# Optimization experiments

Measured on AMD Instinct MI355X. Metric: run time of the kernel, lower is better.

The kernel has to match this reference:

```python
import jax, jax.numpy as jnp
import numpy as np

EPS = 1e-12

def _l2n(x):
    return x / jnp.sqrt(jnp.maximum(jnp.sum(x * x, axis=-1, keepdims=True), EPS))

def _sn_kernel(w, u):
    # One power iteration of spectral normalization (TF SpectralNormalization._compute_weights).
    wr = w.reshape(-1, w.shape[-1])           # [in, out] (1x1 conv kernel flattened)
    v = _l2n(u @ wr.T)                        # [1, in]
    u2 = _l2n(v @ wr)                         # [1, out]
    u2 = jax.lax.stop_gradient(u2)
    v = jax.lax.stop_gradient(v)
    sigma = (v @ wr) @ u2.T                   # [1, 1]
    return w / sigma[0, 0]

def setup_inputs() -> dict:
    key = jax.random.key(0)
    ks = jax.random.split(key, 14)
    B, H, W, C = 8, 64, 64, 256
    d = C // 8
    inp = {
        'x':  jax.random.normal(ks[0], (B, H, W, C), jnp.float32),
        'wf': jax.random.normal(ks[1], (C, d), jnp.float32) * 0.02,
        'bf': jax.random.normal(ks[2], (d,), jnp.float32) * 0.02,
        'uf': jax.random.normal(ks[3], (1, d), jnp.float32) * 0.02,
        'wg': jax.random.normal(ks[4], (C, d), jnp.float32) * 0.02,
        'bg': jax.random.normal(ks[5], (d,), jnp.float32) * 0.02,
        'ug': jax.random.normal(ks[6], (1, d), jnp.float32) * 0.02,
        'wh': jax.random.normal(ks[7], (C, d), jnp.float32) * 0.02,
        'bh': jax.random.normal(ks[8], (d,), jnp.float32) * 0.02,
        'uh': jax.random.normal(ks[9], (1, d), jnp.float32) * 0.02,
        'wv': jax.random.normal(ks[10], (d, C), jnp.float32) * 0.02,
        'bv': jax.random.normal(ks[11], (C,), jnp.float32) * 0.02,
        'uv': jax.random.normal(ks[12], (1, C), jnp.float32) * 0.02,
        'gamma': jax.random.normal(ks[13], (1,), jnp.float32) * 0.1,
    }
    return inp

def reference(x, wf, bf, uf, wg, bg, ug, wh, bh, uh, wv, bv, uv, gamma):
    B, H, W, C = x.shape
    N = H * W
    # spectrally-normalized 1x1 conv kernels
    kf = _sn_kernel(wf, uf)
    kg = _sn_kernel(wg, ug)
    kh = _sn_kernel(wh, uh)
    kv = _sn_kernel(wv, uv)
    # 1x1 convs == channel matmuls on flattened spatial dims
    xf = x.reshape(B, N, C)
    f = xf @ kf + bf            # [B, N, d]
    g = xf @ kg + bg            # [B, N, d]
    h = xf @ kh + bh            # [B, N, d]
    s = jnp.einsum('bnd,bmd->bnm', g, f)   # [B, N, N]
    beta = jax.nn.softmax(s, axis=-1)
    v = jnp.einsum('bnm,bmd->bnd', beta, h)  # [B, N, d]
    o = v @ kv + bv             # [B, N, C]
    out = gamma[0] * o.reshape(B, H, W, C) + x
    return out
```

## Files before the change

### kernel.cpp

```cpp
#include <hip/hip_runtime.h>
#include <math.h>

typedef __attribute__((ext_vector_type(8))) short bf16x8;
typedef __attribute__((ext_vector_type(4))) short bf16x4;
typedef __attribute__((ext_vector_type(4))) float f32x4;

#define LOG2E 1.4426950408889634f

#if __has_builtin(__builtin_amdgcn_exp2f)
#define EXP2(x) __builtin_amdgcn_exp2f(x)
#else
#define EXP2(x) exp2f(x)
#endif

static __device__ __forceinline__ short f2bf(float f) {
  unsigned u = __builtin_bit_cast(unsigned, f);
  u = u + 0x7FFFu + ((u >> 16) & 1u);
  return (short)(u >> 16);
}

__global__ __launch_bounds__(256) void prep_weights(
    const float* __restrict__ wf, const float* __restrict__ wg,
    const float* __restrict__ wh, const float* __restrict__ wv,
    const float* __restrict__ uf, const float* __restrict__ ug,
    const float* __restrict__ uh, const float* __restrict__ uv,
    short* __restrict__ Wt, short* __restrict__ Kvt) {
  __shared__ float sv[256];
  __shared__ float red[256];
  int blk = blockIdx.x;
  int tid = threadIdx.x;
  int sel = (blk < 96) ? (blk >> 5) : 3;
  const float* w = (sel == 0) ? wf : (sel == 1) ? wg : (sel == 2) ? wh : wv;
  const float* u = (sel == 0) ? uf : (sel == 1) ? ug : (sel == 2) ? uh : uv;
  int IN = (sel < 3) ? 256 : 32;
  int OUT = (sel < 3) ? 32 : 256;

  float t = 0.f;
  if (tid < IN) {
    for (int j = 0; j < OUT; j++) t += u[j] * w[tid * OUT + j];
  }
  red[tid] = t * t;
  __syncthreads();
  for (int st = 128; st > 0; st >>= 1) {
    if (tid < st) red[tid] += red[tid + st];
    __syncthreads();
  }
  float nv = sqrtf(fmaxf(red[0], 1e-12f));
  sv[tid] = (tid < IN) ? t / nv : 0.f;
  __syncthreads();

  float s2 = 0.f;
  if (tid < OUT) {
    float sum = 0.f;
    for (int i = 0; i < IN; i++) sum += sv[i] * w[i * OUT + tid];
    s2 = sum * sum;
  }
  red[tid] = s2;
  __syncthreads();
  for (int st = 128; st > 0; st >>= 1) {
    if (tid < st) red[tid] += red[tid + st];
    __syncthreads();
  }
  float sum2 = red[0];
  float sigma = sum2 / sqrtf(fmaxf(sum2, 1e-12f));
  float scale = 1.0f / sigma;
  if (sel == 1) scale *= LOG2E;

  int idx = blk * 256 + tid;
  if (blk < 96) {
    int c = blk, k = tid;
    int cc = c & 31;
    Wt[idx] = f2bf(w[k * 32 + cc] * scale);
  } else {
    int i2 = idx - 96 * 256;
    int c = i2 >> 5, k = i2 & 31;
    Kvt[i2] = f2bf(wv[k * 256 + c] * scale);
  }
}

__global__ __launch_bounds__(256) void proj_kernel(
    const float* __restrict__ x, const short* __restrict__ Wt,
    const float* __restrict__ bf_, const float* __restrict__ bg_,
    const float* __restrict__ bh_, short* __restrict__ fo,
    short* __restrict__ go, short* __restrict__ hto) {
  __shared__ __align__(16) short xs[64][264];
  __shared__ float hsh[64][33];
  int row0 = blockIdx.x * 64;
  int tid = threadIdx.x;
  int wave = tid >> 6;
  int lane = tid & 63;
  int quad = lane >> 4, l16 = lane & 15;
  int rbase = row0 + wave * 16;

  const float4* xb = (const float4*)(x + (size_t)row0 * 256);
#pragma unroll
  for (int i = 0; i < 16; i++) {
    int e4 = i * 256 + tid;
    float4 v = xb[e4];
    int e = e4 * 4;
    int r = e >> 8, c = e & 255;
    bf16x4 s4;
    s4[0] = f2bf(v.x); s4[1] = f2bf(v.y); s4[2] = f2bf(v.z); s4[3] = f2bf(v.w);
    *(bf16x4*)&xs[r][c] = s4;
  }
  __syncthreads();

  f32x4 acc[6];
#pragma unroll
  for (int t = 0; t < 6; t++) acc[t] = (f32x4){0.f, 0.f, 0.f, 0.f};

#pragma unroll
  for (int kc = 0; kc < 256; kc += 32) {
    bf16x8 af = *(const bf16x8*)&xs[wave * 16 + l16][kc + quad * 8];
#pragma unroll
    for (int t = 0; t < 6; t++) {
      bf16x8 bfr = *(const bf16x8*)(Wt + (t * 16 + l16) * 256 + kc + quad * 8);
      acc[t] = __builtin_amdgcn_mfma_f32_16x16x32_bf16(af, bfr, acc[t], 0, 0, 0);
    }
  }

  int b = row0 >> 12;
  int n0 = row0 & 4095;
#pragma unroll
  for (int t = 0; t < 4; t++) {
    int c = t * 16 + l16;
    int sel = c >> 5, cc = c & 31;
    float bb = sel ? (bg_[cc] * LOG2E) : bf_[cc];
    short* dst = sel ? go : fo;
#pragma unroll
    for (int r = 0; r < 4; r++) {
      int row = rbase + quad * 4 + r;
      dst[(size_t)row * 32 + cc] = f2bf(acc[t][r] + bb);
    }
  }
#pragma unroll
  for (int t = 4; t < 6; t++) {
    int cc = (t - 4) * 16 + l16;
    float bb = bh_[cc];
#pragma unroll
    for (int r = 0; r < 4; r++) {
      hsh[wave * 16 + quad * 4 + r][cc] = acc[t][r] + bb;
    }
  }
  __syncthreads();
  {
    int d = threadIdx.x >> 3, ng = threadIdx.x & 7;
    bf16x8 tmp;
#pragma unroll
    for (int i = 0; i < 8; i++) tmp[i] = f2bf(hsh[ng * 8 + i][d]);
    *(bf16x8*)(hto + (size_t)(b * 32 + d) * 4096 + n0 + ng * 8) = tmp;
  }
}

__global__ __launch_bounds__(256, 4) void attn_kernel(
    const short* __restrict__ g_, const short* __restrict__ f_,
    const short* __restrict__ ht_, short* __restrict__ po,
    float* __restrict__ ls) {
  __shared__ __align__(16) short psh[4][4][16][72];
  int b = blockIdx.y;
  int z = blockIdx.z;
  int wave = threadIdx.x >> 6;
  int lane = threadIdx.x & 63;
  int quad = lane >> 4, l16 = lane & 15;
  int qbase = blockIdx.x * 256 + wave * 64;
  int kc0 = z * 512;

  const short* fb = f_ + (size_t)b * 4096 * 32;
  const short* hb = ht_ + (size_t)b * 32 * 4096;

  bf16x8 ga[4];
#pragma unroll
  for (int grp = 0; grp < 4; grp++)
    ga[grp] = *(const bf16x8*)(g_ + (size_t)(b * 4096 + qbase + grp * 16 + l16) * 32 +
                               quad * 8);

  f32x4 oacc[4][2];
  f32x4 lacc[4];
#pragma unroll
  for (int grp = 0; grp < 4; grp++) {
#pragma unroll
    for (int dt = 0; dt < 2; dt++) oacc[grp][dt] = (f32x4){0.f, 0.f, 0.f, 0.f};
    lacc[grp] = (f32x4){0.f, 0.f, 0.f, 0.f};
  }

  short onev = (l16 == 0) ? (short)0x3F80 : (short)0;
  bf16x8 aones = {onev, onev, onev, onev, onev, onev, onev, onev};

  for (int kc = kc0; kc < kc0 + 512; kc += 64) {
    bf16x8 F[4];
#pragma unroll
    for (int t = 0; t < 4; t++)
      F[t] = *(const bf16x8*)(fb + (size_t)(kc + t * 16 + l16) * 32 + quad * 8);
    bf16x8 H[2][2];
#pragma unroll
    for (int half = 0; half < 2; half++)
#pragma unroll
      for (int dt = 0; dt < 2; dt++)
        H[half][dt] = *(const bf16x8*)(hb + (size_t)(dt * 16 + l16) * 4096 +
                                       kc + half * 32 + quad * 8);

#pragma unroll
    for (int g = 0; g < 4; g++) {
      f32x4 s[4];
#pragma unroll
      for (int t = 0; t < 4; t++)
        s[t] = __builtin_amdgcn_mfma_f32_16x16x32_bf16(
            F[t], ga[g], (f32x4){0.f, 0.f, 0.f, 0.f}, 0, 0, 0);

      unsigned long long* prow64 = (unsigned long long*)&psh[wave][g][l16][0];
#pragma unroll
      for (int t = 0; t < 4; t++) {
        float p0 = EXP2(s[t][0]);
        float p1 = EXP2(s[t][1]);
        float p2 = EXP2(s[t][2]);
        float p3 = EXP2(s[t][3]);
        unsigned lo = __builtin_amdgcn_perm(__builtin_bit_cast(unsigned, p1),
                                            __builtin_bit_cast(unsigned, p0),
                                            0x07060302u);
        unsigned hi = __builtin_amdgcn_perm(__builtin_bit_cast(unsigned, p3),
                                            __builtin_bit_cast(unsigned, p2),
                                            0x07060302u);
        prow64[4 * t + quad] = ((unsigned long long)hi << 32) | lo;
      }
      asm volatile("" ::: "memory");

#pragma unroll
      for (int half = 0; half < 2; half++) {
        bf16x8 pa = *(const bf16x8*)(&psh[wave][g][l16][half * 32 + quad * 8]);
#pragma unroll
        for (int dt = 0; dt < 2; dt++)
          oacc[g][dt] = __builtin_amdgcn_mfma_f32_16x16x32_bf16(
              H[half][dt], pa, oacc[g][dt], 0, 0, 0);
        lacc[g] = __builtin_amdgcn_mfma_f32_16x16x32_bf16(aones, pa, lacc[g],
                                                          0, 0, 0);
      }
      asm volatile("" ::: "memory");
    }
  }

#pragma unroll
  for (int grp = 0; grp < 4; grp++) {
    size_t row = (size_t)b * 4096 + qbase + grp * 16 + l16;
    short* pod = po + ((size_t)z * 32768 + row) * 32;
#pragma unroll
    for (int dt = 0; dt < 2; dt++) {
      unsigned w0 = (unsigned)(unsigned short)f2bf(oacc[grp][dt][0]) |
                    ((unsigned)(unsigned short)f2bf(oacc[grp][dt][1]) << 16);
      unsigned w1 = (unsigned)(unsigned short)f2bf(oacc[grp][dt][2]) |
                    ((unsigned)(unsigned short)f2bf(oacc[grp][dt][3]) << 16);
      unsigned* dst = (unsigned*)(pod + dt * 16 + quad * 4);
      dst[0] = w0;
      dst[1] = w1;
    }
  }
  if (quad == 0) {
#pragma unroll
    for (int grp = 0; grp < 4; grp++)
      ls[(size_t)z * 32768 + (size_t)b * 4096 + qbase + grp * 16 + l16] =
          lacc[grp][0];
  }
}

__global__ __launch_bounds__(256) void outproj_kernel(
    const short* __restrict__ po, const float* __restrict__ ls,
    const short* __restrict__ Kvt, const float* __restrict__ bv,
    const float* __restrict__ gamma, const float* __restrict__ x,
    float* __restrict__ out) {
  __shared__ __align__(16) float osh[4][16][260];
  int row0 = blockIdx.x * 64;
  int wave = threadIdx.x >> 6, lane = threadIdx.x & 63;
  int quad = lane >> 4, l16 = lane & 15;
  int rbase = row0 + wave * 16;
  size_t row = (size_t)rbase + l16;

  float vacc[8];
#pragma unroll
  for (int j = 0; j < 8; j++) vacc[j] = 0.f;
  float l = 0.f;
#pragma unroll
  for (int z = 0; z < 8; z++) {
    const unsigned* p =
        (const unsigned*)(po + ((size_t)z * 32768 + row) * 32 + quad * 8);
#pragma unroll
    for (int j = 0; j < 4; j++) {
      unsigned w = p[j];
      vacc[2 * j] += __builtin_bit_cast(float, w << 16);
      vacc[2 * j + 1] += __builtin_bit_cast(float, w & 0xFFFF0000u);
    }
    l += ls[(size_t)z * 32768 + row];
  }
  float inv = 1.0f / l;
  bf16x8 va;
#pragma unroll
  for (int j = 0; j < 8; j++) va[j] = f2bf(vacc[j] * inv);

  float gm = gamma[0];

  f32x4 acc[16];
#pragma unroll
  for (int t = 0; t < 16; t++) {
    bf16x8 kf = *(const bf16x8*)(Kvt + (t * 16 + l16) * 32 + quad * 8);
    acc[t] = __builtin_amdgcn_mfma_f32_16x16x32_bf16(
        va, kf, (f32x4){0.f, 0.f, 0.f, 0.f}, 0, 0, 0);
  }
#pragma unroll
  for (int t = 0; t < 16; t++) {
    float bb = bv[t * 16 + l16];
#pragma unroll
    for (int r = 0; r < 4; r++) {
      osh[wave][quad * 4 + r][t * 16 + l16] = acc[t][r] + bb;
    }
  }
  asm volatile("" ::: "memory");
  {
    int r_l = lane >> 2, c_l = lane & 3;
    int orow = row0 + wave * 16 + r_l;
    const float* oshr = &osh[wave][r_l][0];
    const float4* xr = (const float4*)(x + (size_t)orow * 256);
    float4* outr = (float4*)(out + (size_t)orow * 256);
#pragma unroll
    for (int i = 0; i < 16; i++) {
      int c4 = c_l + i * 4;
      float4 o4 = *(const float4*)&oshr[c4 * 4];
      float4 xv = xr[c4];
      float4 ov;
      ov.x = gm * o4.x + xv.x;
      ov.y = gm * o4.y + xv.y;
      ov.z = gm * o4.z + xv.z;
      ov.w = gm * o4.w + xv.w;
      outr[c4] = ov;
    }
  }
}

extern "C" void kernel_launch(void* const* d_in, const int* in_sizes, int n_in,
                              void* d_out, int out_size, void* d_ws,
                              size_t ws_size, hipStream_t stream) {
  const float* x = (const float*)d_in[0];
  const float* wf = (const float*)d_in[1];
  const float* bf = (const float*)d_in[2];
  const float* uf = (const float*)d_in[3];
  const float* wg = (const float*)d_in[4];
  const float* bg = (const float*)d_in[5];
  const float* ug = (const float*)d_in[6];
  const float* wh = (const float*)d_in[7];
  const float* bh = (const float*)d_in[8];
  const float* uh = (const float*)d_in[9];
  const float* wv = (const float*)d_in[10];
  const float* bv = (const float*)d_in[11];
  const float* uv = (const float*)d_in[12];
  const float* gamma = (const float*)d_in[13];
  float* out = (float*)d_out;

  char* ws = (char*)d_ws;
  short* Wt = (short*)(ws + 1024);
  short* Kvt = (short*)(ws + 64 * 1024);
  short* fo = (short*)(ws + 2u * 1024 * 1024);
  short* go = (short*)(ws + 4u * 1024 * 1024);
  short* hto = (short*)(ws + 6u * 1024 * 1024);
  short* po = (short*)(ws + 10u * 1024 * 1024);
  float* lsp = (float*)(ws + 26u * 1024 * 1024);

  prep_weights<<<128, 256, 0, stream>>>(wf, wg, wh, wv, uf, ug, uh, uv, Wt, Kvt);
  proj_kernel<<<512, 256, 0, stream>>>(x, Wt, bf, bg, bh, fo, go, hto);
  attn_kernel<<<dim3(16, 8, 8), 256, 0, stream>>>(go, fo, hto, po, lsp);
  outproj_kernel<<<512, 256, 0, stream>>>(po, lsp, Kvt, bv, gamma, x, out);
}
```

Baseline: 188.6 us.

## Fuse spectral-norm weight prep into projection and output kernels

Removes the separate prep_weights launch by having every block of the projection and output-projection kernels recompute the spectral-norm power iteration and build the scaled bf16 weight tile in shared memory. The projection kernel also loads x straight into registers as MFMA A-fragments instead of staging it in LDS, and reads weights from a swizzled LDS layout. This saves one kernel launch and a global round trip for the weights. In exchange, each of the 1024 blocks does redundant norm reductions and weight transposition, with extra barriers.

```diff
diff --git a/kernel.cpp b/kernel.cpp
--- a/kernel.cpp
+++ b/kernel.cpp
@@ -19,114 +19,116 @@
   return (short)(u >> 16);
 }
 
-__global__ __launch_bounds__(256) void prep_weights(
-    const float* __restrict__ wf, const float* __restrict__ wg,
-    const float* __restrict__ wh, const float* __restrict__ wv,
-    const float* __restrict__ uf, const float* __restrict__ ug,
-    const float* __restrict__ uh, const float* __restrict__ uv,
-    short* __restrict__ Wt, short* __restrict__ Kvt) {
-  __shared__ float sv[256];
-  __shared__ float red[256];
-  int blk = blockIdx.x;
+__global__ __launch_bounds__(256) void proj_fused(
+    const float* __restrict__ x,
+    const float* __restrict__ wf, const float* __restrict__ bf_,
+    const float* __restrict__ uf,
+    const float* __restrict__ wg, const float* __restrict__ bg_,
+    const float* __restrict__ ug,
+    const float* __restrict__ wh, const float* __restrict__ bh_,
+    const float* __restrict__ uh,
+    short* __restrict__ fo, short* __restrict__ go, short* __restrict__ hto) {
+  __shared__ __align__(16) short wt[96 * 256];
+  __shared__ float scl[3];
   int tid = threadIdx.x;
-  int sel = (blk < 96) ? (blk >> 5) : 3;
-  const float* w = (sel == 0) ? wf : (sel == 1) ? wg : (sel == 2) ? wh : wv;
-  const float* u = (sel == 0) ? uf : (sel == 1) ? ug : (sel == 2) ? uh : uv;
-  int IN = (sel < 3) ? 256 : 32;
-  int OUT = (sel < 3) ? 32 : 256;
-
-  float t = 0.f;
-  if (tid < IN) {
-    for (int j = 0; j < OUT; j++) t += u[j] * w[tid * OUT + j];
-  }
-  red[tid] = t * t;
+  int wave = tid >> 6, lane = tid & 63;
+  int quad = lane >> 4, l16 = lane & 15;
+  int row0 = blockIdx.x * 64;
+
+  const float* xr = x + (size_t)(row0 + wave * 16 + l16) * 256 + quad * 8;
+  bf16x8 afv[8];
+#pragma unroll
+  for (int k8 = 0; k8 < 8; k8++) {
+    float4 a0 = *(const float4*)(xr + k8 * 32);
+    float4 a1 = *(const float4*)(xr + k8 * 32 + 4);
+    bf16x8 a;
+    a[0] = f2bf(a0.x); a[1] = f2bf(a0.y); a[2] = f2bf(a0.z); a[3] = f2bf(a0.w);
+    a[4] = f2bf(a1.x); a[5] = f2bf(a1.y); a[6] = f2bf(a1.z); a[7] = f2bf(a1.w);
+    afv[k8] = a;
+  }
+
+  float* red = (float*)wt;
+  float* sv = (float*)wt + 256;
+#pragma unroll 1
+  for (int sel = 0; sel < 3; sel++) {
+    const float* w = (sel == 0) ? wf : (sel == 1) ? wg : wh;
+    const float* u = (sel == 0) ? uf : (sel == 1) ? ug : uh;
+    float t = 0.f;
+#pragma unroll
+    for (int j = 0; j < 32; j++) t += u[j] * w[tid * 32 + j];
+    float v2 = t * t;
+#pragma unroll
+    for (int off = 32; off > 0; off >>= 1) v2 += __shfl_xor(v2, off);
+    if (lane == 0) red[wave] = v2;
+    __syncthreads();
+    float nv = sqrtf(fmaxf(red[0] + red[1] + red[2] + red[3], 1e-12f));
+    sv[tid] = t / nv;
+    __syncthreads();
+    int c = tid & 31, part = tid >> 5;
+    float p = 0.f;
+#pragma unroll
+    for (int k = 0; k < 32; k++) {
+      int i = part * 32 + k;
+      p += sv[i] * w[i * 32 + c];
+    }
+    red[tid] = p;
+    __syncthreads();
+    float q2 = 0.f;
+    if (tid < 32) {
+      float s_c = 0.f;
+#pragma unroll
+      for (int pp = 0; pp < 8; pp++) s_c += red[tid + 32 * pp];
+      q2 = s_c * s_c;
+    }
+#pragma unroll
+    for (int off = 32; off > 0; off >>= 1) q2 += __shfl_xor(q2, off);
+    if (tid == 0) {
+      float s2 = q2;
+      float sig = s2 / sqrtf(fmaxf(s2, 1e-12f));
+      float s = 1.0f / sig;
+      if (sel == 1) s *= LOG2E;
+      scl[sel] = s;
+    }
+    __syncthreads();
+  }
+
+  float s0 = scl[0], s1 = scl[1], s2v = scl[2];
+#pragma unroll 1
+  for (int c0 = 0; c0 < 96; c0++) {
+    int se = c0 >> 5, cc = c0 & 31;
+    const float* w = (se == 0) ? wf : (se == 1) ? wg : wh;
+    float sc_ = (se == 0) ? s0 : (se == 1) ? s1 : s2v;
+    wt[c0 * 256 + (tid ^ ((c0 & 15) << 3))] = f2bf(w[tid * 32 + cc] * sc_);
+  }
   __syncthreads();
-  for (int st = 128; st > 0; st >>= 1) {
-    if (tid < st) red[tid] += red[tid + st];
-    __syncthreads();
-  }
-  float nv = sqrtf(fmaxf(red[0], 1e-12f));
-  sv[tid] = (tid < IN) ? t / nv : 0.f;
+
+  f32x4 acc[6];
+#pragma unroll
+  for (int t = 0; t < 6; t++) acc[t] = (f32x4){0.f, 0.f, 0.f, 0.f};
+#pragma unroll
+  for (int k8 = 0; k8 < 8; k8++) {
+    int kc = k8 * 32;
+#pragma unroll
+    for (int t = 0; t < 6; t++) {
+      int rw = t * 16 + l16;
+      bf16x8 bfr =
+          *(const bf16x8*)&wt[rw * 256 + ((kc + quad * 8) ^ (l16 << 3))];
+      acc[t] =
+          __builtin_amdgcn_mfma_f32_16x16x32_bf16(afv[k8], bfr, acc[t], 0, 0, 0);
+    }
+  }
   __syncthreads();
 
-  float s2 = 0.f;
-  if (tid < OUT) {
-    float sum = 0.f;
-    for (int i = 0; i < IN; i++) sum += sv[i] * w[i * OUT + tid];
-    s2 = sum * sum;
-  }
-  red[tid] = s2;
-  __syncthreads();
-  for (int st = 128; st > 0; st >>= 1) {
-    if (tid < st) red[tid] += red[tid + st];
-    __syncthreads();
-  }
-  float sum2 = red[0];
-  float sigma = sum2 / sqrtf(fmaxf(sum2, 1e-12f));
-  float scale = 1.0f / sigma;
-  if (sel == 1) scale *= LOG2E;
-
-  int idx = blk * 256 + tid;
-  if (blk < 96) {
-    int c = blk, k = tid;
-    int cc = c & 31;
-    Wt[idx] = f2bf(w[k * 32 + cc] * scale);
-  } else {
-    int i2 = idx - 96 * 256;
-    int c = i2 >> 5, k = i2 & 31;
-    Kvt[i2] = f2bf(wv[k * 256 + c] * scale);
-  }
-}
-
-__global__ __launch_bounds__(256) void proj_kernel(
-    const float* __restrict__ x, const short* __restrict__ Wt,
-    const float* __restrict__ bf_, const float* __restrict__ bg_,
-    const float* __restrict__ bh_, short* __restrict__ fo,
-    short* __restrict__ go, short* __restrict__ hto) {
-  __shared__ __align__(16) short xs[64][264];
-  __shared__ float hsh[64][33];
-  int row0 = blockIdx.x * 64;
-  int tid = threadIdx.x;
-  int wave = tid >> 6;
-  int lane = tid & 63;
-  int quad = lane >> 4, l16 = lane & 15;
-  int rbase = row0 + wave * 16;
-
-  const float4* xb = (const float4*)(x + (size_t)row0 * 256);
-#pragma unroll
-  for (int i = 0; i < 16; i++) {
-    int e4 = i * 256 + tid;
-    float4 v = xb[e4];
-    int e = e4 * 4;
-    int r = e >> 8, c = e & 255;
-    bf16x4 s4;
-    s4[0] = f2bf(v.x); s4[1] = f2bf(v.y); s4[2] = f2bf(v.z); s4[3] = f2bf(v.w);
-    *(bf16x4*)&xs[r][c] = s4;
-  }
-  __syncthreads();
-
-  f32x4 acc[6];
-#pragma unroll
-  for (int t = 0; t < 6; t++) acc[t] = (f32x4){0.f, 0.f, 0.f, 0.f};
-
-#pragma unroll
-  for (int kc = 0; kc < 256; kc += 32) {
-    bf16x8 af = *(const bf16x8*)&xs[wave * 16 + l16][kc + quad * 8];
-#pragma unroll
-    for (int t = 0; t < 6; t++) {
-      bf16x8 bfr = *(const bf16x8*)(Wt + (t * 16 + l16) * 256 + kc + quad * 8);
-      acc[t] = __builtin_amdgcn_mfma_f32_16x16x32_bf16(af, bfr, acc[t], 0, 0, 0);
-    }
-  }
-
+  float* hsh = (float*)wt;
   int b = row0 >> 12;
   int n0 = row0 & 4095;
+  int rbase = row0 + wave * 16;
 #pragma unroll
   for (int t = 0; t < 4; t++) {
     int c = t * 16 + l16;
-    int sel = c >> 5, cc = c & 31;
-    float bb = sel ? (bg_[cc] * LOG2E) : bf_[cc];
-    short* dst = sel ? go : fo;
+    int se = c >> 5, cc = c & 31;
+    float bb = se ? (bg_[cc] * LOG2E) : bf_[cc];
+    short* dst = se ? go : fo;
 #pragma unroll
     for (int r = 0; r < 4; r++) {
       int row = rbase + quad * 4 + r;
@@ -138,16 +140,15 @@
     int cc = (t - 4) * 16 + l16;
     float bb = bh_[cc];
 #pragma unroll
-    for (int r = 0; r < 4; r++) {
-      hsh[wave * 16 + quad * 4 + r][cc] = acc[t][r] + bb;
-    }
+    for (int r = 0; r < 4; r++)
+      hsh[(wave * 16 + quad * 4 + r) * 33 + cc] = acc[t][r] + bb;
   }
   __syncthreads();
   {
-    int d = threadIdx.x >> 3, ng = threadIdx.x & 7;
+    int d = tid >> 3, ng = tid & 7;
     bf16x8 tmp;
 #pragma unroll
-    for (int i = 0; i < 8; i++) tmp[i] = f2bf(hsh[ng * 8 + i][d]);
+    for (int i = 0; i < 8; i++) tmp[i] = f2bf(hsh[(ng * 8 + i) * 33 + d]);
     *(bf16x8*)(hto + (size_t)(b * 32 + d) * 4096 + n0 + ng * 8) = tmp;
   }
 }
@@ -261,15 +262,64 @@
   }
 }
 
-__global__ __launch_bounds__(256) void outproj_kernel(
+__global__ __launch_bounds__(256) void outproj_fused(
     const short* __restrict__ po, const float* __restrict__ ls,
-    const short* __restrict__ Kvt, const float* __restrict__ bv,
-    const float* __restrict__ gamma, const float* __restrict__ x,
-    float* __restrict__ out) {
+    const float* __restrict__ wv, const float* __restrict__ uv,
+    const float* __restrict__ bv, const float* __restrict__ gamma,
+    const float* __restrict__ x, float* __restrict__ out) {
   __shared__ __align__(16) float osh[4][16][260];
+  short* kv = (short*)osh;
+  float* redp = (float*)((char*)osh + 20480);
+  float* svv = (float*)((char*)osh + 21504);
+  float* sclv = (float*)((char*)osh + 21632);
+  int tid = threadIdx.x;
+  int wave = tid >> 6, lane = tid & 63;
+  int quad = lane >> 4, l16 = lane & 15;
+
+  {
+    int i = tid >> 3, p8 = tid & 7;
+    float pv = 0.f;
+#pragma unroll
+    for (int k = 0; k < 32; k++) {
+      int j = p8 * 32 + k;
+      pv += uv[j] * wv[i * 256 + j];
+    }
+    redp[tid] = pv;
+    __syncthreads();
+    float vi = 0.f;
+    if (tid < 32) {
+#pragma unroll
+      for (int p = 0; p < 8; p++) vi += redp[tid * 8 + p];
+    }
+    float q2 = (tid < 32) ? vi * vi : 0.f;
+#pragma unroll
+    for (int off = 32; off > 0; off >>= 1) q2 += __shfl_xor(q2, off);
+    if (tid == 0) sclv[0] = sqrtf(fmaxf(q2, 1e-12f));
+    __syncthreads();
+    if (tid < 32) svv[tid] = vi / sclv[0];
+    __syncthreads();
+    float yc = 0.f;
+#pragma unroll
+    for (int i2 = 0; i2 < 32; i2++) yc += svv[i2] * wv[i2 * 256 + tid];
+    float q3 = yc * yc;
+#pragma unroll
+    for (int off = 32; off > 0; off >>= 1) q3 += __shfl_xor(q3, off);
+    if (lane == 0) redp[wave] = q3;
+    __syncthreads();
+    if (tid == 0) {
+      float s2 = redp[0] + redp[1] + redp[2] + redp[3];
+      float sig = s2 / sqrtf(fmaxf(s2, 1e-12f));
+      sclv[1] = 1.0f / sig;
+    }
+    __syncthreads();
+    float scv = sclv[1];
+#pragma unroll
+    for (int i2 = 0; i2 < 32; i2++)
+      kv[tid * 40 + i2] = f2bf(wv[i2 * 256 + tid] * scv);
+  }
+  __syncthreads();
+
   int row0 = blockIdx.x * 64;
-  int wave = threadIdx.x >> 6, lane = threadIdx.x & 63;
-  int quad = lane >> 4, l16 = lane & 15;
   int rbase = row0 + wave * 16;
   size_t row = (size_t)rbase + l16;
 
@@ -299,10 +349,12 @@
   f32x4 acc[16];
 #pragma unroll
   for (int t = 0; t < 16; t++) {
-    bf16x8 kf = *(const bf16x8*)(Kvt + (t * 16 + l16) * 32 + quad * 8);
+    bf16x8 kf = *(const bf16x8*)&kv[(t * 16 + l16) * 40 + quad * 8];
     acc[t] = __builtin_amdgcn_mfma_f32_16x16x32_bf16(
         va, kf, (f32x4){0.f, 0.f, 0.f, 0.f}, 0, 0, 0);
   }
+  __syncthreads();
+
 #pragma unroll
   for (int t = 0; t < 16; t++) {
     float bb = bv[t * 16 + l16];
@@ -353,16 +405,14 @@
   float* out = (float*)d_out;
 
   char* ws = (char*)d_ws;
-  short* Wt = (short*)(ws + 1024);
-  short* Kvt = (short*)(ws + 64 * 1024);
   short* fo = (short*)(ws + 2u * 1024 * 1024);
   short* go = (short*)(ws + 4u * 1024 * 1024);
   short* hto = (short*)(ws + 6u * 1024 * 1024);
   short* po = (short*)(ws + 10u * 1024 * 1024);
   float* lsp = (float*)(ws + 26u * 1024 * 1024);
 
-  prep_weights<<<128, 256, 0, stream>>>(wf, wg, wh, wv, uf, ug, uh, uv, Wt, Kvt);
-  proj_kernel<<<512, 256, 0, stream>>>(x, Wt, bf, bg, bh, fo, go, hto);
+  proj_fused<<<512, 256, 0, stream>>>(x, wf, bf, uf, wg, bg, ug, wh, bh, uh,
+                                      fo, go, hto);
   attn_kernel<<<dim3(16, 8, 8), 256, 0, stream>>>(go, fo, hto, po, lsp);
-  outproj_kernel<<<512, 256, 0, stream>>>(po, lsp, Kvt, bv, gamma, x, out);
+  outproj_fused<<<512, 256, 0, stream>>>(po, lsp, wv, uv, bv, gamma, x, out);
 }
```

After: 189.9 us. About the same (+0.7%).
